# Optimization experiments

Hardware: AMD Instinct MI355X
Metric: run time of the kernel (lower is better)

Reference implementation:

```python
import jax, jax.numpy as jnp
import numpy as np
import math

B, S, H, NH = 2, 1024, 768, 12
DH = H // NH  # 64

def setup_inputs() -> dict:
    key = jax.random.key(0)
    ks = jax.random.split(key, 8)
    sc = 0.02
    return {
        "hidden_states": jax.random.normal(ks[0], (B, S, H), jnp.float32),
        "bbox_pos_emb": jax.random.normal(ks[1], (S, S, B, DH), jnp.float32),
        "attention_mask": jnp.zeros((B, 1, 1, S), jnp.float32),
        "Wq": jax.random.normal(ks[2], (H, H), jnp.float32) * sc,
        "bq": jnp.zeros((H,), jnp.float32),
        "Wk": jax.random.normal(ks[3], (H, H), jnp.float32) * sc,
        "bk": jnp.zeros((H,), jnp.float32),
        "Wv": jax.random.normal(ks[4], (H, H), jnp.float32) * sc,
        "bv": jnp.zeros((H,), jnp.float32),
    }

def reference(hidden_states, bbox_pos_emb, attention_mask, Wq, bq, Wk, bk, Wv, bv):
    b, s, h = hidden_states.shape
    def proj(W, bias):
        # (b, s, h) -> (b, nh, s, dh)
        y = hidden_states @ W.T + bias
        return y.reshape(b, s, NH, DH).transpose(0, 2, 1, 3)
    q = proj(Wq, bq)
    k = proj(Wk, bk)
    v = proj(Wv, bv)
    # QK^T: (b, nh, s, s)
    scores = jnp.einsum("bnid,bnjd->bnij", q, k)
    # bbox bias: (s, s, b, dh) -> (b, s, s, dh); bnid,bijd->bnij
    bbox = bbox_pos_emb.transpose(2, 0, 1, 3)
    scores = scores + jnp.einsum("bnid,bijd->bnij", q, bbox)
    scores = scores / math.sqrt(DH)
    scores = scores + attention_mask
    probs = jax.nn.softmax(scores, axis=-1)
    ctx = jnp.einsum("bnij,bnjd->bnid", probs, v)
    ctx = ctx.transpose(0, 2, 1, 3).reshape(b, s, h)
    return ctx
```

## Files before the change

### kernel.cpp

```cpp
#include <hip/hip_runtime.h>
#include <hip/hip_bf16.h>

typedef short bf4 __attribute__((ext_vector_type(4)));
typedef short short8 __attribute__((ext_vector_type(8)));
typedef float f32x4 __attribute__((ext_vector_type(4)));

#define MFMA(a, b, c) __builtin_amdgcn_mfma_f32_16x16x32_bf16((a), (b), (c), 0, 0, 0)

#define NB 2
#define NS 1024
#define NHID 768
#define NHEAD 12
#define NDH 64

__device__ __forceinline__ short f2bf(float x) {
    __hip_bfloat16 h = __float2bfloat16(x);
    return *reinterpret_cast<short*>(&h);
}

__device__ __forceinline__ int xcd_swz(int orig, int nwg) {
    return (orig & 7) * (nwg >> 3) + (orig >> 3);
}

typedef const __attribute__((address_space(1))) void gas_t;
typedef __attribute__((address_space(3))) void las_t;
__device__ __forceinline__ void gld_lds16(const float* g, float* l) {
    __builtin_amdgcn_global_load_lds((gas_t*)g, (las_t*)l, 16, 0, 0);
}
__device__ __forceinline__ void gld_lds16s(const short* g, short* l) {
    __builtin_amdgcn_global_load_lds((gas_t*)g, (las_t*)l, 16, 0, 0);
}

#define NHE (2048 * 768)
#define WE  (768 * 768)
__global__ void cvt_bf16_all(
    const float* __restrict__ hidden,
    const float* __restrict__ Wq, const float* __restrict__ Wk,
    const float* __restrict__ Wv,
    short* __restrict__ Xbf, short* __restrict__ Wbf)
{
    const int base = (blockIdx.x * 256 + threadIdx.x) * 4;
    const float* src; short* dst; int off;
    if (base < NHE)               { src = hidden; dst = Xbf;          off = base; }
    else if (base < NHE + WE)     { src = Wq;     dst = Wbf;          off = base - NHE; }
    else if (base < NHE + 2 * WE) { src = Wk;     dst = Wbf + WE;     off = base - NHE - WE; }
    else                          { src = Wv;     dst = Wbf + 2 * WE; off = base - NHE - 2 * WE; }
    f32x4 v = *reinterpret_cast<const f32x4*>(src + off);
    bf4 r;
    r[0] = f2bf(v[0]); r[1] = f2bf(v[1]); r[2] = f2bf(v[2]); r[3] = f2bf(v[3]);
    *reinterpret_cast<bf4*>(dst + off) = r;
}

__global__ __launch_bounds__(256, 3) void qkv_gemm(
    const short* __restrict__ Xbf, const short* __restrict__ Wbf,
    const float* __restrict__ bq, const float* __restrict__ bk,
    const float* __restrict__ bv,
    short* __restrict__ Qo, short* __restrict__ Ko, short* __restrict__ VTo)
{
    const int lane = threadIdx.x & 63;
    const int wave = threadIdx.x >> 6;
    const int lg = lane >> 4, lr = lane & 15;

    const int wgid = xcd_swz(blockIdx.x, 32 * 36);
    const int m0 = (wgid / 36) * 64;
    const int n0 = (wgid % 36) * 64;
    const int proj = n0 / NHID;
    const int ncol0 = n0 % NHID;
    const float* bias = proj == 0 ? bq : (proj == 1 ? bk : bv);

    __shared__ short Alds[3][64 * 64];
    __shared__ short Blds[3][64 * 64];

    f32x4 acc[4];
    #pragma unroll
    for (int s = 0; s < 4; ++s) acc[s] = (f32x4){0.f, 0.f, 0.f, 0.f};

    auto stage = [&](int t, int buf) {
        const int k0 = t * 64;
        #pragma unroll
        for (int p = 0; p < 2; ++p) {
            const int op = wave * 2 + p;
            const int unit = op * 64 + lane;
            const int r = unit >> 3, u = unit & 7;
            const int g = u ^ (r & 7);
            gld_lds16s(Xbf + (size_t)(m0 + r) * NHID + k0 + g * 8,
                       &Alds[buf][op * 512]);
        }
        #pragma unroll
        for (int p = 0; p < 2; ++p) {
            const int op = wave * 2 + p;
            const int unit = op * 64 + lane;
            const int r = unit >> 3, u = unit & 7;
            const int g = u ^ (r & 7);
            gld_lds16s(Wbf + (size_t)(n0 + r) * NHID + k0 + g * 8,
                       &Blds[buf][op * 512]);
        }
    };

    auto compute = [&](int buf) {
        #pragma unroll
        for (int kk = 0; kk < 2; ++kk) {
            const int U = kk * 4 + lg;
            const int Ra = wave * 16 + lr;
            short8 a = *reinterpret_cast<const short8*>(
                &Alds[buf][(Ra * 8 + (U ^ (Ra & 7))) * 8]);
            #pragma unroll
            for (int s = 0; s < 4; ++s) {
                const int R = s * 16 + lr;
                short8 b = *reinterpret_cast<const short8*>(
                    &Blds[buf][(R * 8 + (U ^ (R & 7))) * 8]);
                acc[s] = MFMA(a, b, acc[s]);
            }
        }
    };

    stage(0, 0);
    for (int t = 0; t < 12; ++t) {
        if (t < 11) {
            stage(t + 1, (t + 1) % 3);
            asm volatile("s_waitcnt vmcnt(4)" ::: "memory");
        } else {
            asm volatile("s_waitcnt vmcnt(0)" ::: "memory");
        }
        __builtin_amdgcn_s_barrier();
        compute(t % 3);
    }

    #pragma unroll
    for (int s = 0; s < 4; ++s) {
        const int ncol = ncol0 + s * 16 + lr;
        const float badd = bias[ncol];
        #pragma unroll
        for (int r = 0; r < 4; ++r) {
            const int m = m0 + wave * 16 + lg * 4 + r;
            const short v16 = f2bf(acc[s][r] + badd);
            if (proj == 0) {
                Qo[(size_t)m * NHID + ncol] = v16;
            } else if (proj == 1) {
                Ko[(size_t)m * NHID + ncol] = v16;
            } else {
                const int b = m >> 10, ss = m & 1023;
                const int h = ncol >> 6, dd = ncol & 63;
                VTo[(((size_t)(b * NHEAD + h) * NDH + dd) << 10) + ss] = v16;
            }
        }
    }
}

__global__ __launch_bounds__(256, 2) void bias_gemm(
    const short* __restrict__ Q,
    const float* __restrict__ bbox,
    const float* __restrict__ mask,
    short* __restrict__ biasH)
{
    const int lane = threadIdx.x & 63;
    const int wave = threadIdx.x >> 6;
    const int lg = lane >> 4, lr = lane & 15;
    const int i = blockIdx.x;
    const int jq = wave * 256;

    __shared__ float lds[4][2][2048];

    short8 qa[2][2];
    #pragma unroll
    for (int b2 = 0; b2 < 2; ++b2)
        #pragma unroll
        for (int kk = 0; kk < 2; ++kk)
            qa[b2][kk] = *reinterpret_cast<const short8*>(
                Q + ((size_t)(b2 * NS) + i) * NHID + lr * 64 + kk * 32 + lg * 8);

    const int r_half = lane >> 5;
    const int u_lin = lane & 31;

    auto stage = [&](int t, int buf) {
        const int j0 = jq + t * 16;
        float* dst = &lds[wave][buf][0];
        #pragma unroll
        for (int w = 0; w < 8; ++w) {
            const int r = 2 * w + r_half;
            const int u = u_lin ^ (r & 7);
            const float* src = bbox + (size_t)(i * NS + j0 + r) * 128 + u * 4;
            gld_lds16(src, dst + w * 256);
        }
    };

    auto compute = [&](int t, int buf) {
        const float* tile = &lds[wave][buf][0];
        const int j0 = jq + t * 16;
        const int x = lr & 7;
        #pragma unroll
        for (int b2 = 0; b2 < 2; ++b2) {
            const float mk = mask[b2 * NS + j0 + lr];
            f32x4 c = (f32x4){0.f, 0.f, 0.f, 0.f};
            #pragma unroll
            for (int kk = 0; kk < 2; ++kk) {
                const int q0 = b2 * 16 + kk * 8 + lg * 2;
                f32x4 ca = *reinterpret_cast<const f32x4*>(tile + (size_t)(lr * 32 + ((q0)     ^ x)) * 4);
                f32x4 cb = *reinterpret_cast<const f32x4*>(tile + (size_t)(lr * 32 + ((q0 + 1) ^ x)) * 4);
                short8 bf;
                bf[0] = f2bf(ca[0]); bf[1] = f2bf(ca[1]); bf[2] = f2bf(ca[2]); bf[3] = f2bf(ca[3]);
                bf[4] = f2bf(cb[0]); bf[5] = f2bf(cb[1]); bf[6] = f2bf(cb[2]); bf[7] = f2bf(cb[3]);
                c = MFMA(qa[b2][kk], bf, c);
            }
            if (lg < 3) {
                #pragma unroll
                for (int r = 0; r < 4; ++r) {
                    const int n = lg * 4 + r;
                    biasH[((size_t)(b2 * NHEAD + n) * NS + i) * NS + j0 + lr] =
                        f2bf(c[r] * 0.125f + mk);
                }
            }
        }
    };

    stage(0, 0);
    for (int t = 0; t < 16; ++t) {
        const int buf = t & 1;
        asm volatile("s_waitcnt lgkmcnt(0)" ::: "memory");
        if (t < 15) stage(t + 1, buf ^ 1);
        if (t == 0 || t == 15) asm volatile("s_waitcnt vmcnt(8)"  ::: "memory");
        else                   asm volatile("s_waitcnt vmcnt(16)" ::: "memory");
        compute(t, buf);
    }
}

__global__ __launch_bounds__(256, 3) void attn3(
    const short* __restrict__ Q,
    const short* __restrict__ K,
    const short* __restrict__ VT,
    const short* __restrict__ biasH,
    float* __restrict__ out)
{
    const int tid = threadIdx.x;
    const int lane = tid & 63;
    const int wave = tid >> 6;
    const int lg = lane >> 4, lr = lane & 15;

    const int wgid = xcd_swz(blockIdx.x, 24 * 16);
    const int bh = wgid >> 4;
    const int ic = wgid & 15;
    const int b = bh / NHEAD, h = bh % NHEAD;
    const int i0 = ic * 64 + wave * 16;

    __shared__ short Klds[3][2048];
    __shared__ short Vlds[3][2048];
    __shared__ short Blds[3][2048];
    __shared__ short plds[4][16 * 40];

    short8 qa[2];
    #pragma unroll
    for (int kk = 0; kk < 2; ++kk)
        qa[kk] = *reinterpret_cast<const short8*>(
            Q + ((size_t)(b * NS) + i0 + lr) * NHID + h * 64 + kk * 32 + lg * 8);

    const short* Kb = K + (size_t)b * NS * NHID + h * 64;
    const short* Vb = VT + (size_t)(b * NHEAD + h) * NDH * NS;
    const short* Bb = biasH + ((size_t)(b * NHEAD + h) * NS + ic * 64) * NS;

    f32x4 ctx[4];
    #pragma unroll
    for (int dt = 0; dt < 4; ++dt) ctx[dt] = (f32x4){0.f, 0.f, 0.f, 0.f};
    f32x4 den = (f32x4){0.f, 0.f, 0.f, 0.f};

    const int kr = tid >> 3, ku = tid & 7;
    const int kgu = ku ^ (kr & 7);
    const int vr = tid >> 2, vu = tid & 3;
    const int vgu = vu ^ (vr & 3);
    const int br = tid >> 2, bu = tid & 3;

    auto stage = [&](int t, int buf) {
        const int j0 = t * 32;
        gld_lds16s(Kb + (size_t)(j0 + kr) * NHID + kgu * 8, &Klds[buf][tid * 8]);
        gld_lds16s(Vb + (size_t)vr * NS + j0 + vgu * 8,     &Vlds[buf][tid * 8]);
        gld_lds16s(Bb + (size_t)br * NS + j0 + bu * 8,      &Blds[buf][tid * 8]);
    };

    auto compute = [&](int buf) {
        f32x4 sc[2];
        #pragma unroll
        for (int s = 0; s < 2; ++s) {
            f32x4 c = (f32x4){0.f, 0.f, 0.f, 0.f};
            #pragma unroll
            for (int kk = 0; kk < 2; ++kk) {
                const int R = s * 16 + lr;
                const int U = kk * 4 + lg;
                short8 kf = *reinterpret_cast<const short8*>(
                    &Klds[buf][(R * 8 + (U ^ (R & 7))) * 8]);
                c = MFMA(qa[kk], kf, c);
            }
            sc[s] = c;
        }
        #pragma unroll
        for (int s = 0; s < 2; ++s)
            #pragma unroll
            for (int r = 0; r < 4; ++r) {
                const unsigned int u = (unsigned int)(unsigned short)
                    Blds[buf][wave * 512 + (lg * 4 + r) * 32 + s * 16 + lr] << 16;
                float bb;
                __builtin_memcpy(&bb, &u, 4);
                sc[s][r] = __expf(sc[s][r] * 0.125f + bb);
            }
        den += sc[0] + sc[1];

        #pragma unroll
        for (int s = 0; s < 2; ++s)
            #pragma unroll
            for (int r = 0; r < 4; ++r)
                plds[wave][(lg * 4 + r) * 40 + s * 16 + lr] = f2bf(sc[s][r]);
        asm volatile("" ::: "memory");
        short8 pa = *reinterpret_cast<const short8*>(&plds[wave][lr * 40 + lg * 8]);
        asm volatile("" ::: "memory");

        #pragma unroll
        for (int dt = 0; dt < 4; ++dt) {
            const int R = dt * 16 + lr;
            short8 vf = *reinterpret_cast<const short8*>(
                &Vlds[buf][(R * 4 + (lg ^ (R & 3))) * 8]);
            ctx[dt] = MFMA(pa, vf, ctx[dt]);
        }
    };

    stage(0, 0);
    for (int t = 0; t < 32; ++t) {
        if (t < 31) {
            stage(t + 1, (t + 1) % 3);
            asm volatile("s_waitcnt vmcnt(3)" ::: "memory");
        } else {
            asm volatile("s_waitcnt vmcnt(0)" ::: "memory");
        }
        __builtin_amdgcn_s_barrier();
        compute(t % 3);
    }

    #pragma unroll
    for (int w = 1; w < 16; w <<= 1) {
        f32x4 o;
        #pragma unroll
        for (int r = 0; r < 4; ++r) o[r] = __shfl_xor(den[r], w, 64);
        den += o;
    }

    #pragma unroll
    for (int r = 0; r < 4; ++r) {
        const float inv = 1.0f / den[r];
        const int i = i0 + lg * 4 + r;
        #pragma unroll
        for (int dt = 0; dt < 4; ++dt)
            out[((size_t)(b * NS) + i) * NHID + h * 64 + dt * 16 + lr] =
                ctx[dt][r] * inv;
    }
}

extern "C" void kernel_launch(void* const* d_in, const int* in_sizes, int n_in,
                              void* d_out, int out_size, void* d_ws, size_t ws_size,
                              hipStream_t stream) {
    (void)in_sizes; (void)n_in; (void)out_size; (void)ws_size;
    const float* hidden = (const float*)d_in[0];
    const float* bbox   = (const float*)d_in[1];
    const float* mask   = (const float*)d_in[2];
    const float* Wq = (const float*)d_in[3]; const float* bq = (const float*)d_in[4];
    const float* Wk = (const float*)d_in[5]; const float* bk = (const float*)d_in[6];
    const float* Wv = (const float*)d_in[7]; const float* bv = (const float*)d_in[8];
    float* out = (float*)d_out;

    char* ws = (char*)d_ws;
    const size_t qkv_bytes = (size_t)NB * NS * NHID * sizeof(short);
    short* Qw  = (short*)ws;
    short* Kw  = (short*)(ws + qkv_bytes);
    short* VTw = (short*)(ws + 2 * qkv_bytes);
    short* biasH = (short*)(ws + 3 * qkv_bytes);
    const size_t bias_bytes = (size_t)NB * NHEAD * NS * NS * sizeof(short);
    short* Xbf = (short*)(ws + 3 * qkv_bytes + bias_bytes);
    short* Wbf = Xbf + (size_t)2048 * NHID;

    const int cvt_total = (NHE + 3 * WE) / 4;
    cvt_bf16_all<<<cvt_total / 256, 256, 0, stream>>>(hidden, Wq, Wk, Wv, Xbf, Wbf);

    qkv_gemm<<<32 * 36, 256, 0, stream>>>(Xbf, Wbf, bq, bk, bv, Qw, Kw, VTw);

    bias_gemm<<<NS, 256, 0, stream>>>(Qw, bbox, mask, biasH);

    attn3<<<24 * 16, 256, 0, stream>>>(Qw, Kw, VTw, biasH, out);
}
```

Before: 207.9 us.

## Split QKV GEMM: compute Q first, overlap K/V GEMM with bbox bias kernel

The QKV projection is split so that only the Q projection runs first. The K and V projection tiles are then folded into the bbox bias kernel as extra heterogeneous blocks, interleaved 4 bias blocks to 3 KV blocks. This hides the K/V GEMM behind the memory-bound bbox streaming and removes one serialized launch phase. The cost is a larger shared-memory footprint per block (64KB union) and occupancy capped by the bias kernel's launch bounds for the GEMM tiles.

```diff
diff --git a/kernel.cpp b/kernel.cpp
--- a/kernel.cpp
+++ b/kernel.cpp
@@ -51,25 +51,21 @@
     *reinterpret_cast<bf4*>(dst + off) = r;
 }
 
-__global__ __launch_bounds__(256, 3) void qkv_gemm(
+__device__ __forceinline__ void qkv_block(
+    int m0, int n0,
     const short* __restrict__ Xbf, const short* __restrict__ Wbf,
     const float* __restrict__ bq, const float* __restrict__ bk,
     const float* __restrict__ bv,
-    short* __restrict__ Qo, short* __restrict__ Ko, short* __restrict__ VTo)
+    short* __restrict__ Qo, short* __restrict__ Ko, short* __restrict__ VTo,
+    short (*Alds)[4096], short (*Blds)[4096])
 {
     const int lane = threadIdx.x & 63;
     const int wave = threadIdx.x >> 6;
     const int lg = lane >> 4, lr = lane & 15;
 
-    const int wgid = xcd_swz(blockIdx.x, 32 * 36);
-    const int m0 = (wgid / 36) * 64;
-    const int n0 = (wgid % 36) * 64;
     const int proj = n0 / NHID;
     const int ncol0 = n0 % NHID;
     const float* bias = proj == 0 ? bq : (proj == 1 ? bk : bv);
-
-    __shared__ short Alds[3][64 * 64];
-    __shared__ short Blds[3][64 * 64];
 
     f32x4 acc[4];
     #pragma unroll
@@ -147,19 +143,18 @@
     }
 }
 
-__global__ __launch_bounds__(256, 2) void bias_gemm(
+__device__ __forceinline__ void bias_block(
+    int i,
     const short* __restrict__ Q,
     const float* __restrict__ bbox,
     const float* __restrict__ mask,
-    short* __restrict__ biasH)
+    short* __restrict__ biasH,
+    float (*lds)[2][2048])
 {
     const int lane = threadIdx.x & 63;
     const int wave = threadIdx.x >> 6;
     const int lg = lane >> 4, lr = lane & 15;
-    const int i = blockIdx.x;
     const int jq = wave * 256;
-
-    __shared__ float lds[4][2][2048];
 
     short8 qa[2][2];
     #pragma unroll
@@ -224,6 +219,47 @@
     }
 }
 
+__global__ __launch_bounds__(256, 3) void q_gemm(
+    const short* __restrict__ Xbf, const short* __restrict__ Wbf,
+    const float* __restrict__ bq, const float* __restrict__ bk,
+    const float* __restrict__ bv,
+    short* __restrict__ Qo, short* __restrict__ Ko, short* __restrict__ VTo)
+{
+    __shared__ short Alds[3][4096];
+    __shared__ short Blds[3][4096];
+    const int s = xcd_swz(blockIdx.x, 384);
+    const int m0 = (s / 12) * 64;
+    const int n0 = (s % 12) * 64;
+    qkv_block(m0, n0, Xbf, Wbf, bq, bk, bv, Qo, Ko, VTo, Alds, Blds);
+}
+
+__global__ __launch_bounds__(256, 2) void bias_kv(
+    const short* __restrict__ Qw,
+    const float* __restrict__ bbox,
+    const float* __restrict__ mask,
+    short* __restrict__ biasH,
+    const short* __restrict__ Xbf, const short* __restrict__ Wbf,
+    const float* __restrict__ bq, const float* __restrict__ bk,
+    const float* __restrict__ bv,
+    short* __restrict__ Ko, short* __restrict__ VTo)
+{
+    __shared__ __align__(16) char smem[65536];
+    const int bid = blockIdx.x;
+    const int grp = bid / 7, rem = bid % 7;
+    if (rem < 4) {
+        const int i = grp * 4 + rem;
+        bias_block(i, Qw, bbox, mask, biasH, (float(*)[2][2048])smem);
+    } else {
+        const int kvid = grp * 3 + (rem - 4);
+        const int s = xcd_swz(kvid, 768);
+        const int m0 = (s / 24) * 64;
+        const int n0 = NHID + (s % 24) * 64;
+        qkv_block(m0, n0, Xbf, Wbf, bq, bk, bv,
+                  nullptr, Ko, VTo,
+                  (short(*)[4096])smem, (short(*)[4096])(smem + 24576));
+    }
+}
+
 __global__ __launch_bounds__(256, 3) void attn3(
     const short* __restrict__ Q,
     const short* __restrict__ K,
@@ -376,9 +412,10 @@
     const int cvt_total = (NHE + 3 * WE) / 4;
     cvt_bf16_all<<<cvt_total / 256, 256, 0, stream>>>(hidden, Wq, Wk, Wv, Xbf, Wbf);
 
-    qkv_gemm<<<32 * 36, 256, 0, stream>>>(Xbf, Wbf, bq, bk, bv, Qw, Kw, VTw);
-
-    bias_gemm<<<NS, 256, 0, stream>>>(Qw, bbox, mask, biasH);
+    q_gemm<<<384, 256, 0, stream>>>(Xbf, Wbf, bq, bk, bv, Qw, Kw, VTw);
+
+    bias_kv<<<1792, 256, 0, stream>>>(Qw, bbox, mask, biasH,
+                                      Xbf, Wbf, bq, bk, bv, Kw, VTw);
 
     attn3<<<24 * 16, 256, 0, stream>>>(Qw, Kw, VTw, biasH, out);
 }
```

Result: faster. 191.5 us (median of 2 runs) (-7.9%).
